# Performance work log

Measured on AMD Instinct MI355X. Metric: run time of the kernel, lower is better.

Reference implementation:

```python
import jax, jax.numpy as jnp
import numpy as np

D_K = 128.0  # temp_softmax buffer value


def setup_inputs() -> dict:
    key = jax.random.key(0)
    kq, kk, kv = jax.random.split(key, 3)
    B, S, D = 16, 2048, 128
    q = jax.random.normal(kq, (B, S, D), dtype=jnp.float32)
    k = jax.random.normal(kk, (B, S, D), dtype=jnp.float32)
    v = jax.random.normal(kv, (B, S, D), dtype=jnp.float32)
    mask = jnp.zeros((S, S), dtype=jnp.float32)  # additive mask: 0 = keep, -inf = masked
    return {"q": q, "k": k, "v": v, "mask": mask}


def reference(q, k, v, mask):
    # scores: [B, Sq, Sk]
    attn = jnp.einsum('bqd,bkd->bqk', q, k)
    attn = attn / jnp.sqrt(jnp.asarray(D_K, dtype=attn.dtype))  # scale=True
    attn = attn + mask  # broadcast [Sq,Sk] over batch
    attn = jax.nn.softmax(attn, axis=2)
    # dropout=None -> no dropout
    output = jnp.einsum('bqk,bkd->bqd', attn, v)
    return (output, attn)
```

## Files before the change

kernel.cpp:

```cpp
#include <hip/hip_runtime.h>

#define BATCH 16
#define SEQ   2048
#define DH    128
#define BM    64
#define BN    64
#define NT    (SEQ / BN)

typedef float  f32x4 __attribute__((ext_vector_type(4)));
typedef short  s16x8 __attribute__((ext_vector_type(8)));
typedef short  s16x4 __attribute__((ext_vector_type(4)));
typedef unsigned short u16;

__device__ __forceinline__ short f2bf(float f) {
    union { float f; unsigned u; } a; a.f = f;
    unsigned r = a.u + 0x7FFFu + ((a.u >> 16) & 1u);
    return (short)(r >> 16);
}

__device__ __forceinline__ void gl_lds16(const void* g, void* l) {
    __builtin_amdgcn_global_load_lds(
        (const __attribute__((address_space(1))) void*)g,
        (__attribute__((address_space(3))) void*)l, 16, 0, 0);
}

__global__ __launch_bounds__(256)
void conv_qk(const float* __restrict__ q, const float* __restrict__ k,
             const float* __restrict__ mask, u16* __restrict__ qw,
             char* __restrict__ kw, int* __restrict__ flag) {
    size_t e = ((size_t)blockIdx.x * 256 + threadIdx.x) * 8;

    f32x4 f0 = *(const f32x4*)(q + e);
    f32x4 f1 = *(const f32x4*)(q + e + 4);
    s16x8 w;
    w[0]=f2bf(f0[0]); w[1]=f2bf(f0[1]); w[2]=f2bf(f0[2]); w[3]=f2bf(f0[3]);
    w[4]=f2bf(f1[0]); w[5]=f2bf(f1[1]); w[6]=f2bf(f1[2]); w[7]=f2bf(f1[3]);
    *(s16x8*)(qw + e) = w;

    f0 = *(const f32x4*)(k + e);
    f1 = *(const f32x4*)(k + e + 4);
    w[0]=f2bf(f0[0]); w[1]=f2bf(f0[1]); w[2]=f2bf(f0[2]); w[3]=f2bf(f0[3]);
    w[4]=f2bf(f1[0]); w[5]=f2bf(f1[1]); w[6]=f2bf(f1[2]); w[7]=f2bf(f1[3]);
    int    d0   = (int)(e & 127);
    size_t srow = e >> 7;
    int    row  = (int)(srow & 63);
    size_t tile = srow >> 6;
    *(s16x8*)(kw + (tile << 14) +
              ((((row << 8) + (d0 << 1)) ^ ((row & 7) << 4)))) = w;

    f0 = *(const f32x4*)(mask + e);
    f1 = *(const f32x4*)(mask + e + 4);
    bool nz = f0[0]!=0.f || f0[1]!=0.f || f0[2]!=0.f || f0[3]!=0.f ||
              f1[0]!=0.f || f1[1]!=0.f || f1[2]!=0.f || f1[3]!=0.f;
    if (__ballot(nz) != 0ull) {
        if ((threadIdx.x & 63) == 0) atomicOr(flag, 1);
    }
}

__global__ __launch_bounds__(256)
void conv_v(const float* __restrict__ v, char* __restrict__ vw) {
    __shared__ u16 lt[64][132];
    const int tid = threadIdx.x;
    const int kt = blockIdx.x, b = blockIdx.y;
    const float* src = v + (((size_t)b * SEQ + kt * 64) << 7);
    #pragma unroll
    for (int i = 0; i < 8; ++i) {
        int c = i * 256 + tid;
        int j = c >> 5, d0 = (c & 31) * 4;
        f32x4 f = *(const f32x4*)(src + (j << 7) + d0);
        s16x4 w4; w4[0]=f2bf(f[0]); w4[1]=f2bf(f[1]); w4[2]=f2bf(f[2]); w4[3]=f2bf(f[3]);
        *(s16x4*)&lt[j][d0] = w4;
    }
    __syncthreads();
    char* dstt = vw + (((size_t)b * NT + kt) << 14);
    #pragma unroll
    for (int i = 0; i < 4; ++i) {
        int c = i * 256 + tid;
        int d = c >> 3, jg = c & 7;
        s16x8 w8;
        #pragma unroll
        for (int s = 0; s < 8; ++s) w8[s] = (short)lt[jg * 8 + s][d];
        *(s16x8*)(dstt + (((d << 7) + jg * 16) ^ ((d & 7) << 4))) = w8;
    }
}

#define KOFF0 0
#define VOFF0 32768
#define POFF  65536

#define STAGE16K(SRC, LOFF) do {                                   \
    const char* _s = (SRC); const int _o = tid * 16;               \
    gl_lds16(_s + _o,         smem + (LOFF) + _o);                 \
    gl_lds16(_s + _o + 4096,  smem + (LOFF) + _o + 4096);          \
    gl_lds16(_s + _o + 8192,  smem + (LOFF) + _o + 8192);          \
    gl_lds16(_s + _o + 12288, smem + (LOFF) + _o + 12288);         \
} while (0)

__global__ __launch_bounds__(256, 2)
void attn_main(const u16* __restrict__ qw, const char* __restrict__ kw,
               const char* __restrict__ vw, const float* __restrict__ mask,
               const int* __restrict__ flag,
               float* __restrict__ out_o, float* __restrict__ out_p) {
    extern __shared__ char smem[];
    const int tid  = threadIdx.x;
    const int wave = tid >> 6, lane = tid & 63, quad = lane >> 4, l16 = lane & 15;
    const int b = blockIdx.y, q0 = blockIdx.x * BM;
    const float CS  = 0.08838834764831845f * 1.4426950408889634f;
    const float L2E = 1.4426950408889634f;
    const int hm = *flag;
    const int sw   = (l16 & 7) << 4;
    const int kcol = wave * 16 + l16;

    s16x8 aq[4][4];
    #pragma unroll
    for (int mt = 0; mt < 4; ++mt) {
        const u16* qp = qw + ((size_t)(b * SEQ + q0 + mt * 16 + l16) << 7);
        #pragma unroll
        for (int s = 0; s < 4; ++s)
            aq[mt][s] = *(const s16x8*)(qp + s * 32 + quad * 8);
    }

    const char* kb = kw + ((size_t)(b * NT) << 14);
    const char* vb = vw + ((size_t)(b * NT) << 14);

    float lsum[4][4];
    #pragma unroll
    for (int mt = 0; mt < 4; ++mt)
        #pragma unroll
        for (int r = 0; r < 4; ++r) lsum[mt][r] = 0.f;

    STAGE16K(kb, KOFF0);
    __syncthreads();
    int kof = KOFF0;
    for (int kt = 0; kt < NT; ++kt) {
        if (kt + 1 < NT) STAGE16K(kb + ((size_t)(kt + 1) << 14), kof ^ 16384);
        const int j0 = kt * BN;
        s16x8 bk[4];
        #pragma unroll
        for (int s = 0; s < 4; ++s)
            bk[s] = *(const s16x8*)(smem + kof +
                (((kcol << 8) + s * 64 + quad * 16) ^ sw));
        #pragma unroll
        for (int mt = 0; mt < 4; ++mt) {
            f32x4 c = {0.f, 0.f, 0.f, 0.f};
            #pragma unroll
            for (int s = 0; s < 4; ++s)
                c = __builtin_amdgcn_mfma_f32_16x16x32_bf16(aq[mt][s], bk[s], c, 0, 0, 0);
            float mk[4] = {0.f, 0.f, 0.f, 0.f};
            if (hm) {
                #pragma unroll
                for (int r = 0; r < 4; ++r)
                    mk[r] = mask[(size_t)(q0 + mt * 16 + quad * 4 + r) * SEQ + j0 + kcol] * L2E;
            }
            #pragma unroll
            for (int r = 0; r < 4; ++r)
                lsum[mt][r] += exp2f(c[r] * CS + mk[r]);
        }
        __syncthreads();
        kof ^= 16384;
    }

    float* ls = (float*)(smem + POFF);
    #pragma unroll
    for (int mt = 0; mt < 4; ++mt)
        #pragma unroll
        for (int r = 0; r < 4; ++r) {
            float s = lsum[mt][r];
            s += __shfl_xor(s, 1);
            s += __shfl_xor(s, 2);
            s += __shfl_xor(s, 4);
            s += __shfl_xor(s, 8);
            lsum[mt][r] = s;
        }
    if (l16 == 0) {
        #pragma unroll
        for (int mt = 0; mt < 4; ++mt)
            #pragma unroll
            for (int r = 0; r < 4; ++r)
                ls[(mt * 16 + quad * 4 + r) * 4 + wave] = lsum[mt][r];
    }
    __syncthreads();
    float linv[4][4];
    #pragma unroll
    for (int mt = 0; mt < 4; ++mt)
        #pragma unroll
        for (int r = 0; r < 4; ++r) {
            f32x4 t = *(const f32x4*)&ls[(mt * 16 + quad * 4 + r) * 4];
            linv[mt][r] = 1.0f / (t[0] + t[1] + t[2] + t[3]);
        }

    f32x4 acc[4][2];
    #pragma unroll
    for (int amt = 0; amt < 4; ++amt) {
        acc[amt][0] = (f32x4){0.f, 0.f, 0.f, 0.f};
        acc[amt][1] = (f32x4){0.f, 0.f, 0.f, 0.f};
    }

    STAGE16K(kb, KOFF0);
    STAGE16K(vb, VOFF0);
    __syncthreads();
    int bof = 0;
    for (int kt = 0; kt < NT; ++kt) {
        if (kt + 1 < NT) {
            STAGE16K(kb + ((size_t)(kt + 1) << 14), KOFF0 + (bof ^ 16384));
            STAGE16K(vb + ((size_t)(kt + 1) << 14), VOFF0 + (bof ^ 16384));
        }
        const int j0 = kt * BN;
        s16x8 bk[4];
        #pragma unroll
        for (int s = 0; s < 4; ++s)
            bk[s] = *(const s16x8*)(smem + KOFF0 + bof +
                (((kcol << 8) + s * 64 + quad * 16) ^ sw));
        #pragma unroll
        for (int mt = 0; mt < 4; ++mt) {
            f32x4 c = {0.f, 0.f, 0.f, 0.f};
            #pragma unroll
            for (int s = 0; s < 4; ++s)
                c = __builtin_amdgcn_mfma_f32_16x16x32_bf16(aq[mt][s], bk[s], c, 0, 0, 0);
            float mk[4] = {0.f, 0.f, 0.f, 0.f};
            if (hm) {
                #pragma unroll
                for (int r = 0; r < 4; ++r)
                    mk[r] = mask[(size_t)(q0 + mt * 16 + quad * 4 + r) * SEQ + j0 + kcol] * L2E;
            }
            #pragma unroll
            for (int r = 0; r < 4; ++r) {
                float p = exp2f(c[r] * CS + mk[r]) * linv[mt][r];
                __builtin_nontemporal_store(p,
                    &out_p[((size_t)(b * SEQ + q0 + mt * 16 + quad * 4 + r) << 11) + j0 + kcol]);
                const int pr = mt * 16 + quad * 4 + r;
                *(short*)(smem + POFF +
                    (((pr << 7) + (kcol << 1)) ^ ((pr & 7) << 4))) = f2bf(p);
            }
        }
        __builtin_amdgcn_sched_barrier(0);
        asm volatile("s_waitcnt lgkmcnt(0)\n\ts_barrier" ::: "memory");
        __builtin_amdgcn_sched_barrier(0);

        const int vbase = VOFF0 + bof;
        #pragma unroll
        for (int s2 = 0; s2 < 2; ++s2) {
            const s16x8 bv0 = *(const s16x8*)(smem + vbase +
                ((((wave * 32 + l16) << 7) + s2 * 64 + quad * 16) ^ sw));
            const s16x8 bv1 = *(const s16x8*)(smem + vbase +
                ((((wave * 32 + 16 + l16) << 7) + s2 * 64 + quad * 16) ^ sw));
            #pragma unroll
            for (int amt = 0; amt < 4; ++amt) {
                const s16x8 pa = *(const s16x8*)(smem + POFF +
                    ((((amt * 16 + l16) << 7) + s2 * 64 + quad * 16) ^ sw));
                acc[amt][0] = __builtin_amdgcn_mfma_f32_16x16x32_bf16(pa, bv0, acc[amt][0], 0, 0, 0);
                acc[amt][1] = __builtin_amdgcn_mfma_f32_16x16x32_bf16(pa, bv1, acc[amt][1], 0, 0, 0);
            }
        }
        __syncthreads();
        bof ^= 16384;
    }

    #pragma unroll
    for (int amt = 0; amt < 4; ++amt)
        #pragma unroll
        for (int nt = 0; nt < 2; ++nt)
            #pragma unroll
            for (int r = 0; r < 4; ++r)
                __builtin_nontemporal_store(acc[amt][nt][r],
                    &out_o[((size_t)(b * SEQ + q0 + amt * 16 + quad * 4 + r) << 7)
                           + wave * 32 + nt * 16 + l16]);
}

extern "C" void kernel_launch(void* const* d_in, const int* in_sizes, int n_in,
                              void* d_out, int out_size, void* d_ws, size_t ws_size,
                              hipStream_t stream) {
    (void)in_sizes; (void)n_in; (void)out_size; (void)ws_size;
    const float* q    = (const float*)d_in[0];
    const float* k    = (const float*)d_in[1];
    const float* v    = (const float*)d_in[2];
    const float* mask = (const float*)d_in[3];
    float* out_o = (float*)d_out;
    float* out_p = out_o + (size_t)BATCH * SEQ * DH;

    char* ws   = (char*)d_ws;
    u16*  qw   = (u16*)ws;
    char* kw   = ws + ((size_t)8 << 20);
    char* vw   = ws + ((size_t)16 << 20);
    int*  flag = (int*)(ws + ((size_t)24 << 20));

    hipMemsetAsync(flag, 0, 4, stream);
    conv_qk<<<dim3(2048), dim3(256), 0, stream>>>(q, k, mask, qw, kw, flag);
    conv_v<<<dim3(NT, BATCH), dim3(256), 0, stream>>>(v, vw);

    static bool attr_done = false;
    if (!attr_done) {
        (void)hipFuncSetAttribute((const void*)attn_main,
                                  hipFuncAttributeMaxDynamicSharedMemorySize, 73728);
        attr_done = true;
    }
    attn_main<<<dim3(SEQ / BM, BATCH), dim3(256), 73728, stream>>>(
        qw, kw, vw, mask, flag, out_o, out_p);
}
```

Baseline: 399.1 us.

## Halve query tile to 32 rows, single-buffer K/V and raise occupancy to four blocks

Shrinks the per-block query tile from 64 to 32 rows and raises the launch bound to 4 blocks per CU. Shared memory drops from 72 KB to about 37 KB: the second pass now keeps one K and one V buffer, and the P tile moves to padded per-wave strips. The next K tile is prefetched while the PV MFMAs run, and s_setprio is raised around MFMA sections. Together these aim for more resident waves to hide latency. The cost is twice the K/V tile traffic per query row, no double buffering of V, and possibly misaligned 16-byte LDS reads on the 40-byte-stride P strips.

After: 916.8 us. 130% more time.

```diff
diff --git a/kernel.cpp b/kernel.cpp
--- a/kernel.cpp
+++ b/kernel.cpp
@@ -3,7 +3,7 @@
 #define BATCH 16
 #define SEQ   2048
 #define DH    128
-#define BM    64
+#define BM    32
 #define BN    64
 #define NT    (SEQ / BN)
 
@@ -84,9 +84,9 @@
     }
 }
 
-#define KOFF0 0
-#define VOFF0 32768
-#define POFF  65536
+#define KOFF 0
+#define VOFF 16384
+#define POFF 32768
 
 #define STAGE16K(SRC, LOFF) do {                                   \
     const char* _s = (SRC); const int _o = tid * 16;               \
@@ -96,7 +96,7 @@
     gl_lds16(_s + _o + 12288, smem + (LOFF) + _o + 12288);         \
 } while (0)
 
-__global__ __launch_bounds__(256, 2)
+__global__ __launch_bounds__(256, 4)
 void attn_main(const u16* __restrict__ qw, const char* __restrict__ kw,
                const char* __restrict__ vw, const float* __restrict__ mask,
                const int* __restrict__ flag,
@@ -111,9 +111,9 @@
     const int sw   = (l16 & 7) << 4;
     const int kcol = wave * 16 + l16;
 
-    s16x8 aq[4][4];
-    #pragma unroll
-    for (int mt = 0; mt < 4; ++mt) {
+    s16x8 aq[2][4];
+    #pragma unroll
+    for (int mt = 0; mt < 2; ++mt) {
         const u16* qp = qw + ((size_t)(b * SEQ + q0 + mt * 16 + l16) << 7);
         #pragma unroll
         for (int s = 0; s < 4; ++s)
@@ -123,46 +123,55 @@
     const char* kb = kw + ((size_t)(b * NT) << 14);
     const char* vb = vw + ((size_t)(b * NT) << 14);
 
-    float lsum[4][4];
-    #pragma unroll
-    for (int mt = 0; mt < 4; ++mt)
+    float lsum[2][4];
+    #pragma unroll
+    for (int mt = 0; mt < 2; ++mt)
         #pragma unroll
         for (int r = 0; r < 4; ++r) lsum[mt][r] = 0.f;
 
-    STAGE16K(kb, KOFF0);
+    STAGE16K(kb, KOFF);
     __syncthreads();
-    int kof = KOFF0;
+    int kof = 0;
     for (int kt = 0; kt < NT; ++kt) {
         if (kt + 1 < NT) STAGE16K(kb + ((size_t)(kt + 1) << 14), kof ^ 16384);
-        const int j0 = kt * BN;
         s16x8 bk[4];
         #pragma unroll
         for (int s = 0; s < 4; ++s)
             bk[s] = *(const s16x8*)(smem + kof +
                 (((kcol << 8) + s * 64 + quad * 16) ^ sw));
-        #pragma unroll
-        for (int mt = 0; mt < 4; ++mt) {
+        f32x4 cm[2];
+        __builtin_amdgcn_s_setprio(1);
+        #pragma unroll
+        for (int mt = 0; mt < 2; ++mt) {
             f32x4 c = {0.f, 0.f, 0.f, 0.f};
             #pragma unroll
             for (int s = 0; s < 4; ++s)
                 c = __builtin_amdgcn_mfma_f32_16x16x32_bf16(aq[mt][s], bk[s], c, 0, 0, 0);
+            cm[mt] = c;
+        }
+        __builtin_amdgcn_s_setprio(0);
+        #pragma unroll
+        for (int mt = 0; mt < 2; ++mt) {
             float mk[4] = {0.f, 0.f, 0.f, 0.f};
             if (hm) {
                 #pragma unroll
                 for (int r = 0; r < 4; ++r)
-                    mk[r] = mask[(size_t)(q0 + mt * 16 + quad * 4 + r) * SEQ + j0 + kcol] * L2E;
+                    mk[r] = mask[(size_t)(q0 + mt * 16 + quad * 4 + r) * SEQ
+                                 + kt * BN + kcol] * L2E;
             }
             #pragma unroll
             for (int r = 0; r < 4; ++r)
-                lsum[mt][r] += exp2f(c[r] * CS + mk[r]);
+                lsum[mt][r] += exp2f(cm[mt][r] * CS + mk[r]);
         }
         __syncthreads();
         kof ^= 16384;
     }
 
+    STAGE16K(kb, KOFF);
+
     float* ls = (float*)(smem + POFF);
     #pragma unroll
-    for (int mt = 0; mt < 4; ++mt)
+    for (int mt = 0; mt < 2; ++mt)
         #pragma unroll
         for (int r = 0; r < 4; ++r) {
             float s = lsum[mt][r];
@@ -174,90 +183,93 @@
         }
     if (l16 == 0) {
         #pragma unroll
-        for (int mt = 0; mt < 4; ++mt)
+        for (int mt = 0; mt < 2; ++mt)
             #pragma unroll
             for (int r = 0; r < 4; ++r)
                 ls[(mt * 16 + quad * 4 + r) * 4 + wave] = lsum[mt][r];
     }
     __syncthreads();
-    float linv[4][4];
-    #pragma unroll
-    for (int mt = 0; mt < 4; ++mt)
+    float linv[2][4];
+    #pragma unroll
+    for (int mt = 0; mt < 2; ++mt)
         #pragma unroll
         for (int r = 0; r < 4; ++r) {
             f32x4 t = *(const f32x4*)&ls[(mt * 16 + quad * 4 + r) * 4];
             linv[mt][r] = 1.0f / (t[0] + t[1] + t[2] + t[3]);
         }
-
-    f32x4 acc[4][2];
-    #pragma unroll
-    for (int amt = 0; amt < 4; ++amt) {
+    __syncthreads();
+
+    f32x4 acc[2][2];
+    #pragma unroll
+    for (int amt = 0; amt < 2; ++amt) {
         acc[amt][0] = (f32x4){0.f, 0.f, 0.f, 0.f};
         acc[amt][1] = (f32x4){0.f, 0.f, 0.f, 0.f};
     }
 
-    STAGE16K(kb, KOFF0);
-    STAGE16K(vb, VOFF0);
-    __syncthreads();
-    int bof = 0;
     for (int kt = 0; kt < NT; ++kt) {
-        if (kt + 1 < NT) {
-            STAGE16K(kb + ((size_t)(kt + 1) << 14), KOFF0 + (bof ^ 16384));
-            STAGE16K(vb + ((size_t)(kt + 1) << 14), VOFF0 + (bof ^ 16384));
-        }
-        const int j0 = kt * BN;
+        STAGE16K(vb + ((size_t)kt << 14), VOFF);
         s16x8 bk[4];
         #pragma unroll
         for (int s = 0; s < 4; ++s)
-            bk[s] = *(const s16x8*)(smem + KOFF0 + bof +
+            bk[s] = *(const s16x8*)(smem + KOFF +
                 (((kcol << 8) + s * 64 + quad * 16) ^ sw));
-        #pragma unroll
-        for (int mt = 0; mt < 4; ++mt) {
+        f32x4 cm[2];
+        __builtin_amdgcn_s_setprio(1);
+        #pragma unroll
+        for (int mt = 0; mt < 2; ++mt) {
             f32x4 c = {0.f, 0.f, 0.f, 0.f};
             #pragma unroll
             for (int s = 0; s < 4; ++s)
                 c = __builtin_amdgcn_mfma_f32_16x16x32_bf16(aq[mt][s], bk[s], c, 0, 0, 0);
+            cm[mt] = c;
+        }
+        __builtin_amdgcn_s_setprio(0);
+        #pragma unroll
+        for (int mt = 0; mt < 2; ++mt) {
             float mk[4] = {0.f, 0.f, 0.f, 0.f};
             if (hm) {
                 #pragma unroll
                 for (int r = 0; r < 4; ++r)
-                    mk[r] = mask[(size_t)(q0 + mt * 16 + quad * 4 + r) * SEQ + j0 + kcol] * L2E;
+                    mk[r] = mask[(size_t)(q0 + mt * 16 + quad * 4 + r) * SEQ
+                                 + kt * BN + kcol] * L2E;
             }
             #pragma unroll
             for (int r = 0; r < 4; ++r) {
-                float p = exp2f(c[r] * CS + mk[r]) * linv[mt][r];
+                float p = exp2f(cm[mt][r] * CS + mk[r]) * linv[mt][r];
                 __builtin_nontemporal_store(p,
-                    &out_p[((size_t)(b * SEQ + q0 + mt * 16 + quad * 4 + r) << 11) + j0 + kcol]);
+                    &out_p[((size_t)(b * SEQ + q0 + mt * 16 + quad * 4 + r) << 11)
+                           + kt * BN + kcol]);
                 const int pr = mt * 16 + quad * 4 + r;
-                *(short*)(smem + POFF +
-                    (((pr << 7) + (kcol << 1)) ^ ((pr & 7) << 4))) = f2bf(p);
+                *(short*)(smem + POFF + wave * 1280 + pr * 40 + (l16 << 1)) = f2bf(p);
             }
         }
-        __builtin_amdgcn_sched_barrier(0);
-        asm volatile("s_waitcnt lgkmcnt(0)\n\ts_barrier" ::: "memory");
-        __builtin_amdgcn_sched_barrier(0);
-
-        const int vbase = VOFF0 + bof;
+        __syncthreads();
+
+        if (kt + 1 < NT)
+            STAGE16K(kb + ((size_t)(kt + 1) << 14), KOFF);
+
+        __builtin_amdgcn_s_setprio(1);
         #pragma unroll
         for (int s2 = 0; s2 < 2; ++s2) {
-            const s16x8 bv0 = *(const s16x8*)(smem + vbase +
+            const s16x8 bv0 = *(const s16x8*)(smem + VOFF +
                 ((((wave * 32 + l16) << 7) + s2 * 64 + quad * 16) ^ sw));
-            const s16x8 bv1 = *(const s16x8*)(smem + vbase +
+            const s16x8 bv1 = *(const s16x8*)(smem + VOFF +
                 ((((wave * 32 + 16 + l16) << 7) + s2 * 64 + quad * 16) ^ sw));
-            #pragma unroll
-            for (int amt = 0; amt < 4; ++amt) {
-                const s16x8 pa = *(const s16x8*)(smem + POFF +
-                    ((((amt * 16 + l16) << 7) + s2 * 64 + quad * 16) ^ sw));
+            const int strip = s2 * 2 + (quad >> 1);
+            #pragma unroll
+            for (int amt = 0; amt < 2; ++amt) {
+                const s16x8 pa = *(const s16x8*)(smem + POFF + strip * 1280 +
+                    (amt * 16 + l16) * 40 + ((quad & 1) << 4));
                 acc[amt][0] = __builtin_amdgcn_mfma_f32_16x16x32_bf16(pa, bv0, acc[amt][0], 0, 0, 0);
                 acc[amt][1] = __builtin_amdgcn_mfma_f32_16x16x32_bf16(pa, bv1, acc[amt][1], 0, 0, 0);
             }
         }
+        __builtin_amdgcn_s_setprio(0);
         __syncthreads();
-        bof ^= 16384;
-    }
-
-    #pragma unroll
-    for (int amt = 0; amt < 4; ++amt)
+    }
+
+    #pragma unroll
+    for (int amt = 0; amt < 2; ++amt)
         #pragma unroll
         for (int nt = 0; nt < 2; ++nt)
             #pragma unroll
@@ -288,12 +300,6 @@
     conv_qk<<<dim3(2048), dim3(256), 0, stream>>>(q, k, mask, qw, kw, flag);
     conv_v<<<dim3(NT, BATCH), dim3(256), 0, stream>>>(v, vw);
 
-    static bool attr_done = false;
-    if (!attr_done) {
-        (void)hipFuncSetAttribute((const void*)attn_main,
-                                  hipFuncAttributeMaxDynamicSharedMemorySize, 73728);
-        attr_done = true;
-    }
-    attn_main<<<dim3(SEQ / BM, BATCH), dim3(256), 73728, stream>>>(
+    attn_main<<<dim3(SEQ / BM, BATCH), dim3(256), 37888, stream>>>(
         qw, kw, vw, mask, flag, out_o, out_p);
 }
```

## Write attention probabilities from LDS with vector stores, remap blocks per XCD

Applied to the files above, without the earlier changes.

The attention-probability output is now written after the PV MFMA step. Each wave reads the bf16 P tile back from shared memory and issues 16-byte nontemporal stores of full row segments, replacing the scattered 4-byte stores that were interleaved with the exponentials. Blocks are remapped so that each XCD handles two whole batches, which should improve L2 reuse of K and V. s_setprio is raised around the MFMA sections. The stored probabilities are now bf16-rounded values rather than full fp32, which lowers output precision.

Result: no change. 396.2 us (-0.7%).

```diff
diff --git a/kernel.cpp b/kernel.cpp
--- a/kernel.cpp
+++ b/kernel.cpp
@@ -104,7 +104,12 @@
     extern __shared__ char smem[];
     const int tid  = threadIdx.x;
     const int wave = tid >> 6, lane = tid & 63, quad = lane >> 4, l16 = lane & 15;
-    const int b = blockIdx.y, q0 = blockIdx.x * BM;
+
+    const int lid = blockIdx.y * gridDim.x + blockIdx.x;
+    const int xcd = lid & 7, wi = lid >> 3;
+    const int b  = (xcd << 1) | (wi >> 5);
+    const int q0 = (wi & 31) * BM;
+
     const float CS  = 0.08838834764831845f * 1.4426950408889634f;
     const float L2E = 1.4426950408889634f;
     const int hm = *flag;
@@ -134,27 +139,34 @@
     int kof = KOFF0;
     for (int kt = 0; kt < NT; ++kt) {
         if (kt + 1 < NT) STAGE16K(kb + ((size_t)(kt + 1) << 14), kof ^ 16384);
-        const int j0 = kt * BN;
         s16x8 bk[4];
         #pragma unroll
         for (int s = 0; s < 4; ++s)
             bk[s] = *(const s16x8*)(smem + kof +
                 (((kcol << 8) + s * 64 + quad * 16) ^ sw));
+        __builtin_amdgcn_s_setprio(1);
+        f32x4 cm[4];
         #pragma unroll
         for (int mt = 0; mt < 4; ++mt) {
             f32x4 c = {0.f, 0.f, 0.f, 0.f};
             #pragma unroll
             for (int s = 0; s < 4; ++s)
                 c = __builtin_amdgcn_mfma_f32_16x16x32_bf16(aq[mt][s], bk[s], c, 0, 0, 0);
+            cm[mt] = c;
+        }
+        __builtin_amdgcn_s_setprio(0);
+        #pragma unroll
+        for (int mt = 0; mt < 4; ++mt) {
             float mk[4] = {0.f, 0.f, 0.f, 0.f};
             if (hm) {
                 #pragma unroll
                 for (int r = 0; r < 4; ++r)
-                    mk[r] = mask[(size_t)(q0 + mt * 16 + quad * 4 + r) * SEQ + j0 + kcol] * L2E;
+                    mk[r] = mask[(size_t)(q0 + mt * 16 + quad * 4 + r) * SEQ
+                                 + kt * BN + kcol] * L2E;
             }
             #pragma unroll
             for (int r = 0; r < 4; ++r)
-                lsum[mt][r] += exp2f(c[r] * CS + mk[r]);
+                lsum[mt][r] += exp2f(cm[mt][r] * CS + mk[r]);
         }
         __syncthreads();
         kof ^= 16384;
@@ -205,29 +217,34 @@
             STAGE16K(kb + ((size_t)(kt + 1) << 14), KOFF0 + (bof ^ 16384));
             STAGE16K(vb + ((size_t)(kt + 1) << 14), VOFF0 + (bof ^ 16384));
         }
-        const int j0 = kt * BN;
         s16x8 bk[4];
         #pragma unroll
         for (int s = 0; s < 4; ++s)
             bk[s] = *(const s16x8*)(smem + KOFF0 + bof +
                 (((kcol << 8) + s * 64 + quad * 16) ^ sw));
+        __builtin_amdgcn_s_setprio(1);
+        f32x4 cm[4];
         #pragma unroll
         for (int mt = 0; mt < 4; ++mt) {
             f32x4 c = {0.f, 0.f, 0.f, 0.f};
             #pragma unroll
             for (int s = 0; s < 4; ++s)
                 c = __builtin_amdgcn_mfma_f32_16x16x32_bf16(aq[mt][s], bk[s], c, 0, 0, 0);
+            cm[mt] = c;
+        }
+        __builtin_amdgcn_s_setprio(0);
+        #pragma unroll
+        for (int mt = 0; mt < 4; ++mt) {
             float mk[4] = {0.f, 0.f, 0.f, 0.f};
             if (hm) {
                 #pragma unroll
                 for (int r = 0; r < 4; ++r)
-                    mk[r] = mask[(size_t)(q0 + mt * 16 + quad * 4 + r) * SEQ + j0 + kcol] * L2E;
+                    mk[r] = mask[(size_t)(q0 + mt * 16 + quad * 4 + r) * SEQ
+                                 + kt * BN + kcol] * L2E;
             }
             #pragma unroll
             for (int r = 0; r < 4; ++r) {
-                float p = exp2f(c[r] * CS + mk[r]) * linv[mt][r];
-                __builtin_nontemporal_store(p,
-                    &out_p[((size_t)(b * SEQ + q0 + mt * 16 + quad * 4 + r) << 11) + j0 + kcol]);
+                float p = exp2f(cm[mt][r] * CS + mk[r]) * linv[mt][r];
                 const int pr = mt * 16 + quad * 4 + r;
                 *(short*)(smem + POFF +
                     (((pr << 7) + (kcol << 1)) ^ ((pr & 7) << 4))) = f2bf(p);
@@ -238,6 +255,7 @@
         __builtin_amdgcn_sched_barrier(0);
 
         const int vbase = VOFF0 + bof;
+        __builtin_amdgcn_s_setprio(1);
         #pragma unroll
         for (int s2 = 0; s2 < 2; ++s2) {
             const s16x8 bv0 = *(const s16x8*)(smem + vbase +
@@ -252,6 +270,25 @@
                 acc[amt][1] = __builtin_amdgcn_mfma_f32_16x16x32_bf16(pa, bv1, acc[amt][1], 0, 0, 0);
             }
         }
+        __builtin_amdgcn_s_setprio(0);
+
+        #pragma unroll
+        for (int i = 0; i < 4; ++i) {
+            const int prw = wave * 16 + i * 4 + (lane >> 4);
+            const int pcl = (lane & 15) * 4;
+            s16x4 pw = *(const s16x4*)(smem + POFF +
+                (((prw << 7) + (pcl << 1)) ^ ((prw & 7) << 4)));
+            f32x4 pf;
+            #pragma unroll
+            for (int j = 0; j < 4; ++j) {
+                union { unsigned u; float f; } cv;
+                cv.u = ((unsigned)(unsigned short)pw[j]) << 16;
+                pf[j] = cv.f;
+            }
+            __builtin_nontemporal_store(pf, (f32x4*)
+                &out_p[((size_t)(b * SEQ + q0 + prw) << 11) + kt * BN + pcl]);
+        }
+
         __syncthreads();
         bof ^= 16384;
     }
```
